# Kernel optimization log

Measured on AMD Instinct MI355X. Metric: run time of the kernel, lower is better.

The kernel has to match this reference:

```python
import jax, jax.numpy as jnp
import numpy as np

# TT factorization for fc1: 768 = 4*4*6*8 -> 3072 = 4*6*8*16, ranks (1,12,24,12,1)
# TT factorization for fc2: 3072 = 4*6*8*16 -> 768 = 4*4*6*8, ranks (1,12,24,12,1)
IN_F1, OUT_F1 = (4, 4, 6, 8), (4, 6, 8, 16)
IN_F2, OUT_F2 = (4, 6, 8, 16), (4, 4, 6, 8)
RANKS = (12, 24, 12)


def _core(key, shape, fan_in):
    return jax.random.normal(key, shape, dtype=jnp.float32) * (fan_in ** -0.5)


def make_tt_params(key, in_f, out_f, ranks):
    r = (1,) + tuple(ranks) + (1,)
    ks = jax.random.split(key, 5)
    # boundary cores squeeze the unit rank dims
    g1 = _core(ks[0], (in_f[0], out_f[0], r[1]), in_f[0])              # (i1,o1,r1)
    g2 = _core(ks[1], (r[1], in_f[1], out_f[1], r[2]), r[1] * in_f[1])  # (r1,i2,o2,r2)
    g3 = _core(ks[2], (r[2], in_f[2], out_f[2], r[3]), r[2] * in_f[2])  # (r2,i3,o3,r3)
    g4 = _core(ks[3], (r[3], in_f[3], out_f[3]), r[3] * in_f[3])        # (r3,i4,o4)
    b = jnp.zeros((int(np.prod(out_f)),), dtype=jnp.float32)
    return g1, g2, g3, g4, b


def tt_linear(x2d, g1, g2, g3, g4, bias, in_f):
    # x2d: (N, prod(in_f)) -> (N, prod(out_f))
    z = x2d.reshape((-1,) + tuple(in_f))                  # (b,i1,i2,i3,i4)
    z = jnp.einsum('bijkl,ipr->bjklpr', z, g1)            # (b,i2,i3,i4,o1,r1)
    z = jnp.einsum('bjklpr,rjqs->bklpqs', z, g2)          # (b,i3,i4,o1,o2,r2)
    z = jnp.einsum('bklpqs,sktu->blpqtu', z, g3)          # (b,i4,o1,o2,o3,r3)
    z = jnp.einsum('blpqtu,ulv->bpqtv', z, g4)            # (b,o1,o2,o3,o4)
    return z.reshape(z.shape[0], -1) + bias


def setup_inputs() -> dict:
    key = jax.random.key(0)
    kx, k1, k2 = jax.random.split(key, 3)
    x = jax.random.normal(kx, (2, 2048, 768), dtype=jnp.float32)
    g1a, g1b, g1c, g1d, b1 = make_tt_params(k1, IN_F1, OUT_F1, RANKS)
    g2a, g2b, g2c, g2d, b2 = make_tt_params(k2, IN_F2, OUT_F2, RANKS)
    return {"x": x, "g1a": g1a, "g1b": g1b, "g1c": g1c, "g1d": g1d, "b1": b1,
            "g2a": g2a, "g2b": g2b, "g2c": g2c, "g2d": g2d, "b2": b2}


def reference(x, g1a, g1b, g1c, g1d, b1, g2a, g2b, g2c, g2d, b2):
    B, S, D = x.shape
    h = tt_linear(x.reshape(-1, D), g1a, g1b, g1c, g1d, b1, IN_F1)  # (N, 3072)
    h = jax.nn.gelu(h, approximate=False)  # nn.GELU() default = exact erf
    # dropout: identity in eval mode
    y = tt_linear(h, g2a, g2b, g2c, g2d, b2, IN_F2)                 # (N, 768)
    return y.reshape(B, S, -1)
```

## Files before the change

### kernel.cpp

```cpp
#include <hip/hip_runtime.h>
#include <cstdint>
#include <cstddef>

typedef unsigned short u16;
typedef __attribute__((ext_vector_type(8))) __bf16 bf16x8;
typedef __attribute__((ext_vector_type(4))) float f32x4;

__device__ __forceinline__ u16 f2bf(float f) {
  unsigned u = __float_as_uint(f);
  u += 0x7FFFu + ((u >> 16) & 1u);
  return (u16)(u >> 16);
}

__device__ __forceinline__ float bf2f(u16 h) {
  return __uint_as_float(((unsigned)h) << 16);
}

__device__ __forceinline__ void async16(u16* lds, const u16* g) {
  __builtin_amdgcn_global_load_lds(
      (const __attribute__((address_space(1))) unsigned int*)g,
      (__attribute__((address_space(3))) unsigned int*)lds, 16, 0, 0);
}

__global__ __launch_bounds__(256)
void prep(const float4* __restrict__ x4, ushort4* __restrict__ xb4,
          const float* __restrict__ gA1, const float* __restrict__ gB1,
          const float* __restrict__ gC1, const float* __restrict__ gD1,
          const float* __restrict__ gA2, const float* __restrict__ gB2,
          const float* __restrict__ gC2, const float* __restrict__ gD2,
          float* __restrict__ B12_1, float* __restrict__ B12_2,
          float* __restrict__ C1, float* __restrict__ C2) {
  const int b = blockIdx.x;
  const int tid = threadIdx.x;
  if (b < 3072) {
    int i = b * 256 + tid;
    float4 v = x4[i];
    ushort4 o;
    o.x = f2bf(v.x); o.y = f2bf(v.y); o.z = f2bf(v.z); o.w = f2bf(v.w);
    xb4[i] = o;
    return;
  }
  int idx = (b - 3072) * 256 + tid;
  if (idx < 9216) {
    int e = idx;
    int r2 = e % 24; int t = e / 24;
    int fo12 = t % 24, fi12 = t / 24;
    int i2 = fi12 % 4, i1 = fi12 / 4;
    int o2 = fo12 % 6, o1 = fo12 / 6;
    float s = 0.f;
#pragma unroll
    for (int r1 = 0; r1 < 12; ++r1)
      s += gA1[(i1 * 4 + o1) * 12 + r1] * gB1[((r1 * 4 + i2) * 6 + o2) * 24 + r2];
    B12_1[e] = s;
  } else if (idx < 18432) {
    int e = idx - 9216;
    int r2 = e % 24; int t = e / 24;
    int fo12 = t % 16, fi12 = t / 16;
    int i2 = fi12 % 6, i1 = fi12 / 6;
    int o2 = fo12 % 4, o1 = fo12 / 4;
    float s = 0.f;
#pragma unroll
    for (int r1 = 0; r1 < 12; ++r1)
      s += gA2[(i1 * 4 + o1) * 12 + r1] * gB2[((r1 * 6 + i2) * 4 + o2) * 24 + r2];
    B12_2[e] = s;
  } else if (idx < 165888) {
    int e = idx - 18432;
    int fi34 = e % 48; int t = e / 48;
    int fo34 = t % 128;
    int i3 = fi34 / 8, i4 = fi34 % 8;
    int o3 = fo34 / 16, o4 = fo34 % 16;
    int r2 = t / 128;
    float s = 0.f;
#pragma unroll
    for (int r3 = 0; r3 < 12; ++r3)
      s += gC1[((r2 * 6 + i3) * 8 + o3) * 12 + r3] * gD1[(r3 * 8 + i4) * 16 + o4];
    C1[e] = s;
  } else {
    int e = idx - 165888;
    int fi34 = e % 128; int t = e / 128;
    int fo34 = t % 48;
    int i3 = fi34 / 16, i4 = fi34 % 16;
    int o3 = fo34 / 8, o4 = fo34 % 8;
    int r2 = t / 48;
    float s = 0.f;
#pragma unroll
    for (int r3 = 0; r3 < 12; ++r3)
      s += gC2[((r2 * 8 + i3) * 6 + o3) * 12 + r3] * gD2[(r3 * 16 + i4) * 8 + o4];
    C2[e] = s;
  }
}

template <int FI12, int I34, int O12, int O34, int OG>
__device__ __forceinline__
void tt_expand_body(const float* __restrict__ B12, const float* __restrict__ C34t,
                    u16* __restrict__ Wt, int bx, int by, int tid, float* sB) {
  constexpr int R2 = 24;
  constexpr int Kin = FI12 * I34;
  constexpr int IC = Kin / 8;
  constexpr int I34C = I34 / 8;
  for (int e = tid; e < FI12 * OG * R2; e += 256) {
    int r2 = e % R2; int t = e / R2;
    int f = t % OG; int fi12 = t / OG;
    sB[(fi12 * OG + f) * 25 + r2] = B12[(fi12 * O12 + by * OG + f) * R2 + r2];
  }
  __syncthreads();
  const int t = bx * 256 + tid;
  const int fo34 = t / IC;
  const int ic = t % IC;
  const int fi12 = ic / I34C;
  const int fi34 = (ic % I34C) * 8;

  float acc[OG][8];
#pragma unroll
  for (int f = 0; f < OG; ++f)
#pragma unroll
    for (int k = 0; k < 8; ++k) acc[f][k] = 0.f;

  for (int r2 = 0; r2 < R2; ++r2) {
    const float4* cp = (const float4*)(C34t + ((size_t)(r2 * O34 + fo34) * I34 + fi34));
    float4 c0 = cp[0], c1 = cp[1];
    float c[8] = {c0.x, c0.y, c0.z, c0.w, c1.x, c1.y, c1.z, c1.w};
#pragma unroll
    for (int f = 0; f < OG; ++f) {
      float bb = sB[(fi12 * OG + f) * 25 + r2];
#pragma unroll
      for (int k = 0; k < 8; ++k) acc[f][k] += bb * c[k];
    }
  }
#pragma unroll
  for (int f = 0; f < OG; ++f) {
    int out = (by * OG + f) * O34 + fo34;
    u16 v[8];
#pragma unroll
    for (int k = 0; k < 8; ++k) v[k] = f2bf(acc[f][k]);
    *(uint4*)(Wt + (size_t)out * Kin + fi12 * I34 + fi34) = *(const uint4*)v;
  }
}

__global__ __launch_bounds__(256)
void tt_expand2(const float* __restrict__ B12_1, const float* __restrict__ C1, u16* __restrict__ W1t,
                const float* __restrict__ B12_2, const float* __restrict__ C2, u16* __restrict__ W2t) {
  __shared__ float sB[24 * 4 * 25];
  const int b = blockIdx.x;
  const int tid = threadIdx.x;
  if (b < 288) {
    tt_expand_body<16, 48, 24, 128, 4>(B12_1, C1, W1t, b % 48, b / 48, tid, sB);
  } else {
    int bb = b - 288;
    tt_expand_body<24, 128, 16, 48, 4>(B12_2, C2, W2t, bb % 72, bb / 72, tid, sB);
  }
}

__global__ void reduceN8(const uint4* __restrict__ P, const float* __restrict__ bias,
                         float4* __restrict__ out4, int n8, int zstride8, int nz) {
  int i = blockIdx.x * 256 + threadIdx.x;
  if (i >= n8) return;
  int b0 = (i % 96) * 8;
  float a[8];
#pragma unroll
  for (int k = 0; k < 8; ++k) a[k] = bias[b0 + k];
  for (int s = 0; s < nz; ++s) {
    uint4 u = P[i + s * zstride8];
    const u16* up = (const u16*)&u;
#pragma unroll
    for (int k = 0; k < 8; ++k) a[k] += bf2f(up[k]);
  }
  out4[i * 2]     = (float4){a[0], a[1], a[2], a[3]};
  out4[i * 2 + 1] = (float4){a[4], a[5], a[6], a[7]};
}

template <bool GELU, int MINW>
__global__ __launch_bounds__(256, MINW)
void gemm_bt(const u16* __restrict__ A, const u16* __restrict__ Bt,
             const float* __restrict__ bias, u16* __restrict__ Out,
             int N, int K, int klen, size_t zstride) {
  __shared__ __align__(16) u16 As[2][128 * 32];
  __shared__ __align__(16) u16 Bs[2][128 * 32];
  const int tid = threadIdx.x;
  const int bm = blockIdx.x, bn = blockIdx.y;
  const int wave = tid >> 6, lane = tid & 63;
  const int wm = (wave & 1) * 64, wn = (wave >> 1) * 64;
  const int lr = lane & 15, lq = lane >> 4;

  const int srow = tid >> 2;
  const int scol = (tid & 3) * 8;
  const u16* Ag = A + (size_t)(bm * 128 + srow) * K + scol;
  const u16* Bg = Bt + (size_t)(bn * 128 + srow) * K + scol;
  u16* AsW = &As[0][0] + tid * 8;
  u16* BsW = &Bs[0][0] + tid * 8;

  f32x4 acc[4][4];
#pragma unroll
  for (int i = 0; i < 4; i++)
#pragma unroll
    for (int j = 0; j < 4; j++) acc[i][j] = (f32x4){0.f, 0.f, 0.f, 0.f};

  const int kbeg = blockIdx.z * klen;
  const int nIter = klen >> 5;

  auto stage = [&](int buf, int k0) {
    async16(AsW + buf * 4096,        Ag + k0);
    async16(AsW + buf * 4096 + 2048, Ag + k0 + (size_t)64 * K);
    async16(BsW + buf * 4096,        Bg + k0);
    async16(BsW + buf * 4096 + 2048, Bg + k0 + (size_t)64 * K);
  };
  auto compute = [&](int buf) {
    bf16x8 af[4], bfr[4];
#pragma unroll
    for (int i = 0; i < 4; i++)
      af[i] = *(const bf16x8*)(&As[buf][0] + (wm + i * 16 + lr) * 32 + lq * 8);
#pragma unroll
    for (int j = 0; j < 4; j++)
      bfr[j] = *(const bf16x8*)(&Bs[buf][0] + (wn + j * 16 + lr) * 32 + lq * 8);
#pragma unroll
    for (int i = 0; i < 4; i++)
#pragma unroll
      for (int j = 0; j < 4; j++)
        acc[i][j] = __builtin_amdgcn_mfma_f32_16x16x32_bf16(af[i], bfr[j], acc[i][j], 0, 0, 0);
  };

  stage(0, kbeg);
  for (int it = 0; it < nIter; it += 2) {
    __syncthreads();
    if (it + 1 < nIter) stage(1, kbeg + (it + 1) * 32);
    compute(0);
    __syncthreads();
    if (it + 2 < nIter) stage(0, kbeg + (it + 2) * 32);
    compute(1);
  }

  u16* Op = Out + blockIdx.z * zstride;
  const int r0 = bm * 128 + wm + lq * 4;
  const int c0 = bn * 128 + wn + lr;
  float bv[4];
  if (GELU) {
#pragma unroll
    for (int j = 0; j < 4; j++) bv[j] = bias[c0 + j * 16];
  }
#pragma unroll
  for (int i = 0; i < 4; i++) {
#pragma unroll
    for (int r = 0; r < 4; r++) {
      const size_t rowoff = (size_t)(r0 + i * 16 + r) * N;
#pragma unroll
      for (int j = 0; j < 4; j++) {
        float v = acc[i][j][r];
        if (GELU) {
          v += bv[j];
          v = 0.5f * v * (1.f + erff(v * 0.70710678118654752f));
        }
        Op[rowoff + c0 + j * 16] = f2bf(v);
      }
    }
  }
}

extern "C" void kernel_launch(void* const* d_in, const int* in_sizes, int n_in,
                              void* d_out, int out_size, void* d_ws, size_t ws_size,
                              hipStream_t stream) {
  const float* x   = (const float*)d_in[0];
  const float* g1a = (const float*)d_in[1];
  const float* g1b = (const float*)d_in[2];
  const float* g1c = (const float*)d_in[3];
  const float* g1d = (const float*)d_in[4];
  const float* b1  = (const float*)d_in[5];
  const float* g2a = (const float*)d_in[6];
  const float* g2b = (const float*)d_in[7];
  const float* g2c = (const float*)d_in[8];
  const float* g2d = (const float*)d_in[9];
  const float* b2  = (const float*)d_in[10];
  float* out = (float*)d_out;

  char* ws = (char*)d_ws;
  u16* xb   = (u16*)(ws + 0);
  u16* W1t  = (u16*)(ws + 6291456);
  u16* W2t  = (u16*)(ws + 11010048);
  u16* h    = (u16*)(ws + 15728640);
  u16* Part = (u16*)(ws + 40894464);
  float* B12_1 = (float*)(ws + 40894464);
  float* B12_2 = (float*)(ws + 40894464 + 36864);
  float* C1    = (float*)(ws + 40894464 + 73728);
  float* C2    = (float*)(ws + 40894464 + 663552);

  const int nz = (ws_size >= 40894464ull + 8ull * 6291456ull) ? 8 : 4;

  prep<<<4296, 256, 0, stream>>>((const float4*)x, (ushort4*)xb,
                                 g1a, g1b, g1c, g1d, g2a, g2b, g2c, g2d,
                                 B12_1, B12_2, C1, C2);

  tt_expand2<<<576, 256, 0, stream>>>(B12_1, C1, W1t, B12_2, C2, W2t);

  gemm_bt<true, 3><<<dim3(32, 24, 1), 256, 0, stream>>>(xb, W1t, b1, h, 3072, 768, 768, 0);
  gemm_bt<false, 4><<<dim3(32, 6, nz), 256, 0, stream>>>(h, W2t, nullptr, Part,
                                                         768, 3072, 3072 / nz, 3145728);
  reduceN8<<<1536, 256, 0, stream>>>((const uint4*)Part, b2,
                                     (float4*)out, 393216, 393216, nz);
}
```

Measured before the change: 176.4 us.

## Load B operand directly from global into registers, skipping LDS staging

The B (weight) tile is no longer staged in shared memory. Each wave loads its B fragments with direct vector global loads into register double buffers, while A still goes through async LDS staging. This halves LDS footprint and LDS read traffic, but B rows are fetched redundantly by the two waves sharing a column block and global latency is less hidden. Launch bounds are unified to a minimum of 3 blocks per CU for both GEMMs.

```diff
diff --git a/kernel.cpp b/kernel.cpp
--- a/kernel.cpp
+++ b/kernel.cpp
@@ -169,13 +169,12 @@
   out4[i * 2 + 1] = (float4){a[4], a[5], a[6], a[7]};
 }
 
-template <bool GELU, int MINW>
-__global__ __launch_bounds__(256, MINW)
+template <bool GELU>
+__global__ __launch_bounds__(256, 3)
 void gemm_bt(const u16* __restrict__ A, const u16* __restrict__ Bt,
              const float* __restrict__ bias, u16* __restrict__ Out,
              int N, int K, int klen, size_t zstride) {
   __shared__ __align__(16) u16 As[2][128 * 32];
-  __shared__ __align__(16) u16 Bs[2][128 * 32];
   const int tid = threadIdx.x;
   const int bm = blockIdx.x, bn = blockIdx.y;
   const int wave = tid >> 6, lane = tid & 63;
@@ -185,48 +184,48 @@
   const int srow = tid >> 2;
   const int scol = (tid & 3) * 8;
   const u16* Ag = A + (size_t)(bm * 128 + srow) * K + scol;
-  const u16* Bg = Bt + (size_t)(bn * 128 + srow) * K + scol;
+  const u16* Bg = Bt + (size_t)(bn * 128 + wn + lr) * K + lq * 8;
   u16* AsW = &As[0][0] + tid * 8;
-  u16* BsW = &Bs[0][0] + tid * 8;
 
   f32x4 acc[4][4];
 #pragma unroll
   for (int i = 0; i < 4; i++)
 #pragma unroll
     for (int j = 0; j < 4; j++) acc[i][j] = (f32x4){0.f, 0.f, 0.f, 0.f};
+
+  auto stageA = [&](int buf, int k0) {
+    async16(AsW + buf * 4096,        Ag + k0);
+    async16(AsW + buf * 4096 + 2048, Ag + k0 + (size_t)64 * K);
+  };
+  auto loadB = [&](bf16x8* b, int k0) {
+#pragma unroll
+    for (int j = 0; j < 4; j++)
+      b[j] = *(const bf16x8*)(Bg + (size_t)(j * 16) * K + k0);
+  };
+  auto compute = [&](int buf, const bf16x8* b) {
+    bf16x8 af[4];
+#pragma unroll
+    for (int i = 0; i < 4; i++)
+      af[i] = *(const bf16x8*)(&As[buf][0] + (wm + i * 16 + lr) * 32 + lq * 8);
+#pragma unroll
+    for (int i = 0; i < 4; i++)
+#pragma unroll
+      for (int j = 0; j < 4; j++)
+        acc[i][j] = __builtin_amdgcn_mfma_f32_16x16x32_bf16(af[i], b[j], acc[i][j], 0, 0, 0);
+  };
 
   const int kbeg = blockIdx.z * klen;
   const int nIter = klen >> 5;
-
-  auto stage = [&](int buf, int k0) {
-    async16(AsW + buf * 4096,        Ag + k0);
-    async16(AsW + buf * 4096 + 2048, Ag + k0 + (size_t)64 * K);
-    async16(BsW + buf * 4096,        Bg + k0);
-    async16(BsW + buf * 4096 + 2048, Bg + k0 + (size_t)64 * K);
-  };
-  auto compute = [&](int buf) {
-    bf16x8 af[4], bfr[4];
-#pragma unroll
-    for (int i = 0; i < 4; i++)
-      af[i] = *(const bf16x8*)(&As[buf][0] + (wm + i * 16 + lr) * 32 + lq * 8);
-#pragma unroll
-    for (int j = 0; j < 4; j++)
-      bfr[j] = *(const bf16x8*)(&Bs[buf][0] + (wn + j * 16 + lr) * 32 + lq * 8);
-#pragma unroll
-    for (int i = 0; i < 4; i++)
-#pragma unroll
-      for (int j = 0; j < 4; j++)
-        acc[i][j] = __builtin_amdgcn_mfma_f32_16x16x32_bf16(af[i], bfr[j], acc[i][j], 0, 0, 0);
-  };
-
-  stage(0, kbeg);
+  bf16x8 b0[4], b1[4];
+  stageA(0, kbeg);
+  loadB(b0, kbeg);
   for (int it = 0; it < nIter; it += 2) {
     __syncthreads();
-    if (it + 1 < nIter) stage(1, kbeg + (it + 1) * 32);
-    compute(0);
+    if (it + 1 < nIter) { stageA(1, kbeg + (it + 1) * 32); loadB(b1, kbeg + (it + 1) * 32); }
+    compute(0, b0);
     __syncthreads();
-    if (it + 2 < nIter) stage(0, kbeg + (it + 2) * 32);
-    compute(1);
+    if (it + 2 < nIter) { stageA(0, kbeg + (it + 2) * 32); loadB(b0, kbeg + (it + 2) * 32); }
+    compute(1, b1);
   }
 
   u16* Op = Out + blockIdx.z * zstride;
@@ -290,9 +289,9 @@
 
   tt_expand2<<<576, 256, 0, stream>>>(B12_1, C1, W1t, B12_2, C2, W2t);
 
-  gemm_bt<true, 3><<<dim3(32, 24, 1), 256, 0, stream>>>(xb, W1t, b1, h, 3072, 768, 768, 0);
-  gemm_bt<false, 4><<<dim3(32, 6, nz), 256, 0, stream>>>(h, W2t, nullptr, Part,
-                                                         768, 3072, 3072 / nz, 3145728);
+  gemm_bt<true><<<dim3(32, 24, 1), 256, 0, stream>>>(xb, W1t, b1, h, 3072, 768, 768, 0);
+  gemm_bt<false><<<dim3(32, 6, nz), 256, 0, stream>>>(h, W2t, nullptr, Part,
+                                                      768, 3072, 3072 / nz, 3145728);
   reduceN8<<<1536, 256, 0, stream>>>((const uint4*)Part, b2,
                                      (float4*)out, 393216, 393216, nz);
 }
```

Measured after the change: 210.1 us. 19.1% more time.
